# Performance work log

Hardware: AMD Instinct MI355X
Metric: run time of the kernel (lower is better)

The kernel has to match this reference:

```python
import jax, jax.numpy as jnp
import numpy as np

IN_CH = 64        # in_channels
MOD_H = 512       # modulation_hidden_dim
SIREN_H = 512     # siren_hidden_dim
NUM_PTS = 100
SCALE_INIT = 30.0  # SIREN first-layer frequency scale
N_STRANDS = 1024
NR_LAYERS = 3


def _wn_linear(x, v, g, b):
    # torch weight_norm(dim=0) on Linear: w = g * v / ||v||_row, row-wise over in-dim
    w = v * (g[:, None] / jnp.sqrt(jnp.sum(v * v, axis=1, keepdims=True)))
    return x @ w.T + b


def setup_inputs() -> dict:
    key = jax.random.key(0)
    ks = jax.random.split(key, 16)

    def p(k, shape, scale=0.05):
        return jax.random.normal(k, shape, dtype=jnp.float32) * scale

    inp = {"strand_features": p(ks[0], (N_STRANDS, IN_CH), 1.0)}
    mod_in = [IN_CH, MOD_H + IN_CH, MOD_H + IN_CH]
    for i in range(NR_LAYERS):
        inp[f"mod_v{i}"] = p(ks[1 + i], (MOD_H, mod_in[i]))
        inp[f"mod_g{i}"] = jnp.ones((MOD_H,), jnp.float32)
        inp[f"mod_b{i}"] = jnp.zeros((MOD_H,), jnp.float32)
    siren_in = [1, SIREN_H, SIREN_H]
    for i in range(NR_LAYERS):
        inp[f"siren_v{i}"] = p(ks[4 + i], (SIREN_H, siren_in[i]))
        inp[f"siren_g{i}"] = jnp.ones((SIREN_H,), jnp.float32)
        inp[f"siren_b{i}"] = jnp.zeros((SIREN_H,), jnp.float32)
    inp["dec_v"] = p(ks[7], (3, SIREN_H))
    inp["dec_g"] = jnp.ones((3,), jnp.float32)
    inp["dec_b"] = jnp.zeros((3,), jnp.float32)
    return inp


def reference(strand_features,
              mod_v0, mod_g0, mod_b0,
              mod_v1, mod_g1, mod_b1,
              mod_v2, mod_g2, mod_b2,
              siren_v0, siren_g0, siren_b0,
              siren_v1, siren_g1, siren_b1,
              siren_v2, siren_g2, siren_b2,
              dec_v, dec_g, dec_b):
    mods = [(mod_v0, mod_g0, mod_b0), (mod_v1, mod_g1, mod_b1), (mod_v2, mod_g2, mod_b2)]
    sirens = [(siren_v0, siren_g0, siren_b0), (siren_v1, siren_g1, siren_b1), (siren_v2, siren_g2, siren_b2)]

    n = strand_features.shape[0]
    nv = NUM_PTS - 1  # decode_random_verts=False, decode_direct_xyz=False
    # t = linspace(0,1,num_pts)[0:num_pts-1], shape (N, nv, 1)
    t = jnp.linspace(0.0, 1.0, NUM_PTS, dtype=jnp.float32)[:nv].reshape(1, nv, 1)
    h_siren = jnp.broadcast_to(t, (n, nv, 1))
    z_initial = jnp.broadcast_to(strand_features[:, None, :], (n, nv, IN_CH))  # z_scaling = 1.0
    z = z_initial
    for i in range(NR_LAYERS):
        h_mod = jax.nn.silu(_wn_linear(z, *mods[i]))       # (n, nv, MOD_H)
        s = _wn_linear(h_siren, *sirens[i])                # (n, nv, SIREN_H)
        s = jnp.sin(SCALE_INIT * s) if i == 0 else jnp.sin(s)
        h_siren = (1.0 - h_mod) * s                        # FiLM-style gating
        z = jnp.concatenate([z_initial, h_mod], axis=2)    # (n, nv, IN_CH+MOD_H)
    hair_dir = _wn_linear(h_siren, dec_v, dec_g, dec_b) * 0.01  # (n, nv, 3)
    pred = jnp.cumsum(hair_dir, axis=1)
    start = jnp.zeros((n, 1, 3), jnp.float32)
    return jnp.concatenate([start, pred], axis=1)  # (n, NUM_PTS, 3)
```

## Files before the change

### kernel.cpp

```cpp
#include <hip/hip_runtime.h>
#include <math.h>

#define NS 1024
#define NV 99
#define NPTS 100
#define H 512

typedef __bf16 bf16x8 __attribute__((ext_vector_type(8)));
typedef __bf16 bf16x4 __attribute__((ext_vector_type(4)));
typedef float f32x4 __attribute__((ext_vector_type(4)));

#define GLD_LDS16(gp, lp) __builtin_amdgcn_global_load_lds(                 \
    (const __attribute__((address_space(1))) void*)(gp),                    \
    (__attribute__((address_space(3))) void*)(lp), 16, 0, 0)
#define WAIT_VM0()   __builtin_amdgcn_s_waitcnt(0x0f70)
#define WAIT_LGKM0() __builtin_amdgcn_s_waitcnt(0xc07f)

__global__ __launch_bounds__(256) void k_wnorm(
    const float* __restrict__ mv0, const float* __restrict__ mg0,
    const float* __restrict__ mv1, const float* __restrict__ mg1,
    const float* __restrict__ mv2, const float* __restrict__ mg2,
    const float* __restrict__ sv0, const float* __restrict__ sg0,
    const float* __restrict__ sb0,
    const float* __restrict__ sv1, const float* __restrict__ sg1,
    const float* __restrict__ sv2, const float* __restrict__ sg2,
    const float* __restrict__ dv,  const float* __restrict__ dg,
    float* __restrict__ wnM0, float* __restrict__ wnM1, float* __restrict__ wnM2,
    __bf16* __restrict__ W1s, __bf16* __restrict__ W2s, float* __restrict__ wnD,
    float* __restrict__ s0sin)
{
    const int b = blockIdx.x, tid = threadIdx.x;
    if (b >= 641) {
        int idx = (b - 641) * 256 + tid;
        if (idx < NV * H) {
            int p = idx >> 9, j = idx & 511;
            float v = sv0[j];
            float w = sg0[j] * v * rsqrtf(v * v);
            float t = (float)p / 99.0f;
            s0sin[idx] = __sinf(30.0f * (t * w + sb0[j]));
        }
        return;
    }
    const int rid = b * 4 + (tid >> 6);
    const int lane = tid & 63;
    if (rid >= 2563) return;

    const float* src; const float* g; int len, j;
    float* dstf = nullptr; __bf16* dstb = nullptr;
    if (rid < 512)       { j = rid;        src = mv0 + j*64;  g = mg0; dstf = wnM0 + j*64;  len = 64;  }
    else if (rid < 1024) { j = rid - 512;  src = mv1 + j*576; g = mg1; dstf = wnM1 + j*576; len = 576; }
    else if (rid < 1536) { j = rid - 1024; src = mv2 + j*576; g = mg2; dstf = wnM2 + j*576; len = 576; }
    else if (rid < 2048) { j = rid - 1536; src = sv1 + j*512; g = sg1; dstb = W1s;          len = 512; }
    else if (rid < 2560) { j = rid - 2048; src = sv2 + j*512; g = sg2; dstb = W2s;          len = 512; }
    else                 { j = rid - 2560; src = dv  + j*512; g = dg;  dstf = wnD + j*512;  len = 512; }

    float ss = 0.f;
    for (int k = lane; k < len; k += 64) { float v = src[k]; ss += v * v; }
#pragma unroll
    for (int o = 1; o < 64; o <<= 1) ss += __shfl_xor(ss, o, 64);
    const float sc = g[j] * rsqrtf(ss);

    if (dstb) {
        for (int k = lane; k < len; k += 64) {
            int f  = (j >> 4) * 16 + (k >> 5);
            int el = ((f * 64) + ((k >> 3) & 3) * 16 + (j & 15)) * 8 + (k & 7);
            dstb[el] = (__bf16)(src[k] * sc);
        }
    } else {
        for (int k = lane; k < len; k += 64) dstf[k] = src[k] * sc;
    }
}

__global__ __launch_bounds__(256) void k_mod(
    const float* __restrict__ sf,
    const float* __restrict__ wnM0, const float* __restrict__ mb0,
    const float* __restrict__ wnM1, const float* __restrict__ mb1,
    const float* __restrict__ wnM2, const float* __restrict__ mb2,
    float* __restrict__ onem)
{
    const int g0 = blockIdx.x * 4, tid = threadIdx.x;
    __shared__ float z[4][576];

    for (int idx = tid; idx < 4 * 64; idx += 256)
        z[idx >> 6][idx & 63] = sf[(g0 + (idx >> 6)) * 64 + (idx & 63)];
    __syncthreads();

    float mreg[2][4];
#pragma unroll
    for (int r = 0; r < 2; ++r) {
        const int j = tid + 256 * r;
        const float* wr = wnM0 + j * 64;
        float acc[4] = {0.f, 0.f, 0.f, 0.f};
#pragma unroll
        for (int k = 0; k < 64; k += 4) {
            float4 w = *(const float4*)(wr + k);
#pragma unroll
            for (int g = 0; g < 4; ++g) {
                float4 zv = *(const float4*)&z[g][k];
                acc[g] += zv.x * w.x + zv.y * w.y + zv.z * w.z + zv.w * w.w;
            }
        }
        const float b = mb0[j];
#pragma unroll
        for (int g = 0; g < 4; ++g) {
            float a = acc[g] + b;
            float m = a / (1.f + __expf(-a));
            onem[(g0 + g) * H + j] = 1.f - m;
            mreg[r][g] = m;
        }
    }
    __syncthreads();
#pragma unroll
    for (int r = 0; r < 2; ++r)
#pragma unroll
        for (int g = 0; g < 4; ++g) z[g][64 + tid + 256 * r] = mreg[r][g];
    __syncthreads();

#pragma unroll
    for (int r = 0; r < 2; ++r) {
        const int j = tid + 256 * r;
        const float* wr = wnM1 + j * 576;
        float acc[4] = {0.f, 0.f, 0.f, 0.f};
        for (int k = 0; k < 576; k += 4) {
            float4 w = *(const float4*)(wr + k);
#pragma unroll
            for (int g = 0; g < 4; ++g) {
                float4 zv = *(const float4*)&z[g][k];
                acc[g] += zv.x * w.x + zv.y * w.y + zv.z * w.z + zv.w * w.w;
            }
        }
        const float b = mb1[j];
#pragma unroll
        for (int g = 0; g < 4; ++g) {
            float a = acc[g] + b;
            float m = a / (1.f + __expf(-a));
            onem[NS * H + (g0 + g) * H + j] = 1.f - m;
            mreg[r][g] = m;
        }
    }
    __syncthreads();
#pragma unroll
    for (int r = 0; r < 2; ++r)
#pragma unroll
        for (int g = 0; g < 4; ++g) z[g][64 + tid + 256 * r] = mreg[r][g];
    __syncthreads();

#pragma unroll
    for (int r = 0; r < 2; ++r) {
        const int j = tid + 256 * r;
        const float* wr = wnM2 + j * 576;
        float acc[4] = {0.f, 0.f, 0.f, 0.f};
        for (int k = 0; k < 576; k += 4) {
            float4 w = *(const float4*)(wr + k);
#pragma unroll
            for (int g = 0; g < 4; ++g) {
                float4 zv = *(const float4*)&z[g][k];
                acc[g] += zv.x * w.x + zv.y * w.y + zv.z * w.z + zv.w * w.w;
            }
        }
        const float b = mb2[j];
#pragma unroll
        for (int g = 0; g < 4; ++g) {
            float a = acc[g] + b;
            float m = a / (1.f + __expf(-a));
            onem[2 * NS * H + (g0 + g) * H + j] = 1.f - m;
        }
    }
}

__global__ __launch_bounds__(64, 1) void k_main(
    const __bf16* __restrict__ W1s, const __bf16* __restrict__ W2s,
    const float* __restrict__ wnD, const float* __restrict__ sb1,
    const float* __restrict__ sb2, const float* __restrict__ db,
    const float* __restrict__ s0sin, const float* __restrict__ onem,
    float* __restrict__ dirs)
{
    __shared__ __attribute__((aligned(16))) __bf16 h2p[32][520];
    __shared__ __attribute__((aligned(16))) __bf16 wst[8192];
    const int lane = threadIdx.x;
    const int L = lane & 15, Q = lane >> 4;
    const int base = blockIdx.x * 32;
    const int r0 = base + L, r1 = r0 + 16;
    const int s0 = r0 / 99, p0 = r0 - s0 * 99;
    const int s1 = r1 / 99, p1 = r1 - s1 * 99;

    bf16x8 Bh0[16], Bh1[16];
    {
        const float* omA = onem + s0 * H;
        const float* tsA = s0sin + p0 * H;
        const float* omB = onem + s1 * H;
        const float* tsB = s0sin + p1 * H;
#pragma unroll
        for (int t = 0; t < 16; ++t) {
            const int k0 = t * 32 + Q * 8;
            f32x4 oa = *(const f32x4*)(omA + k0);
            f32x4 ob = *(const f32x4*)(omA + k0 + 4);
            f32x4 ta = *(const f32x4*)(tsA + k0);
            f32x4 tb = *(const f32x4*)(tsA + k0 + 4);
            bf16x8 v;
            v[0] = (__bf16)(oa[0] * ta[0]); v[1] = (__bf16)(oa[1] * ta[1]);
            v[2] = (__bf16)(oa[2] * ta[2]); v[3] = (__bf16)(oa[3] * ta[3]);
            v[4] = (__bf16)(ob[0] * tb[0]); v[5] = (__bf16)(ob[1] * tb[1]);
            v[6] = (__bf16)(ob[2] * tb[2]); v[7] = (__bf16)(ob[3] * tb[3]);
            Bh0[t] = v;
            oa = *(const f32x4*)(omB + k0);
            ob = *(const f32x4*)(omB + k0 + 4);
            ta = *(const f32x4*)(tsB + k0);
            tb = *(const f32x4*)(tsB + k0 + 4);
            v[0] = (__bf16)(oa[0] * ta[0]); v[1] = (__bf16)(oa[1] * ta[1]);
            v[2] = (__bf16)(oa[2] * ta[2]); v[3] = (__bf16)(oa[3] * ta[3]);
            v[4] = (__bf16)(ob[0] * tb[0]); v[5] = (__bf16)(ob[1] * tb[1]);
            v[6] = (__bf16)(ob[2] * tb[2]); v[7] = (__bf16)(ob[3] * tb[3]);
            Bh1[t] = v;
        }
    }

    {
        const float* om1a = onem + NS * H + s0 * H;
        const float* om1b = onem + NS * H + s1 * H;
#pragma unroll 1
        for (int kb = 0; kb < 16; ++kb) {
            const __bf16* gpA = W1s + (size_t)kb * 16384 + (size_t)lane * 8;
            WAIT_LGKM0();
#pragma unroll
            for (int t = 0; t < 16; ++t)
                GLD_LDS16(gpA + t * 512, &wst[t * 512]);
            WAIT_VM0();
            f32x4 a00 = {0.f,0.f,0.f,0.f}, a01 = {0.f,0.f,0.f,0.f};
#pragma unroll
            for (int t = 0; t < 16; ++t) {
                bf16x8 w = *(const bf16x8*)&wst[t * 512 + lane * 8];
                a00 = __builtin_amdgcn_mfma_f32_16x16x32_bf16(w, Bh0[t], a00, 0, 0, 0);
                a01 = __builtin_amdgcn_mfma_f32_16x16x32_bf16(w, Bh1[t], a01, 0, 0, 0);
            }
            const __bf16* gpB = gpA + 16 * 512;
            WAIT_LGKM0();
#pragma unroll
            for (int t = 0; t < 16; ++t)
                GLD_LDS16(gpB + t * 512, &wst[t * 512]);
            WAIT_VM0();
            f32x4 a10 = {0.f,0.f,0.f,0.f}, a11 = {0.f,0.f,0.f,0.f};
#pragma unroll
            for (int t = 0; t < 16; ++t) {
                bf16x8 w = *(const bf16x8*)&wst[t * 512 + lane * 8];
                a10 = __builtin_amdgcn_mfma_f32_16x16x32_bf16(w, Bh0[t], a10, 0, 0, 0);
                a11 = __builtin_amdgcn_mfma_f32_16x16x32_bf16(w, Bh1[t], a11, 0, 0, 0);
            }
            const int c0 = kb * 32 + Q * 4, c1 = c0 + 16;
            float4 bi0 = *(const float4*)(sb1 + c0);
            float4 bi1 = *(const float4*)(sb1 + c1);
            float4 ga0 = *(const float4*)(om1a + c0);
            float4 ga1 = *(const float4*)(om1a + c1);
            float4 gb0 = *(const float4*)(om1b + c0);
            float4 gb1 = *(const float4*)(om1b + c1);
            bf16x4 v;
            v[0] = (__bf16)(ga0.x * __sinf(a00[0] + bi0.x));
            v[1] = (__bf16)(ga0.y * __sinf(a00[1] + bi0.y));
            v[2] = (__bf16)(ga0.z * __sinf(a00[2] + bi0.z));
            v[3] = (__bf16)(ga0.w * __sinf(a00[3] + bi0.w));
            *(bf16x4*)&h2p[L][c0] = v;
            v[0] = (__bf16)(ga1.x * __sinf(a10[0] + bi1.x));
            v[1] = (__bf16)(ga1.y * __sinf(a10[1] + bi1.y));
            v[2] = (__bf16)(ga1.z * __sinf(a10[2] + bi1.z));
            v[3] = (__bf16)(ga1.w * __sinf(a10[3] + bi1.w));
            *(bf16x4*)&h2p[L][c1] = v;
            v[0] = (__bf16)(gb0.x * __sinf(a01[0] + bi0.x));
            v[1] = (__bf16)(gb0.y * __sinf(a01[1] + bi0.y));
            v[2] = (__bf16)(gb0.z * __sinf(a01[2] + bi0.z));
            v[3] = (__bf16)(gb0.w * __sinf(a01[3] + bi0.w));
            *(bf16x4*)&h2p[16 + L][c0] = v;
            v[0] = (__bf16)(gb1.x * __sinf(a11[0] + bi1.x));
            v[1] = (__bf16)(gb1.y * __sinf(a11[1] + bi1.y));
            v[2] = (__bf16)(gb1.z * __sinf(a11[2] + bi1.z));
            v[3] = (__bf16)(gb1.w * __sinf(a11[3] + bi1.w));
            *(bf16x4*)&h2p[16 + L][c1] = v;
        }
    }
    __syncthreads();

#pragma unroll
    for (int t = 0; t < 16; ++t) {
        Bh0[t] = *(const bf16x8*)&h2p[L][t * 32 + Q * 8];
        Bh1[t] = *(const bf16x8*)&h2p[16 + L][t * 32 + Q * 8];
    }

    float pA0 = 0.f, pA1 = 0.f, pA2 = 0.f;
    float pB0 = 0.f, pB1 = 0.f, pB2 = 0.f;
    {
        const float* om2a = onem + 2 * NS * H + s0 * H;
        const float* om2b = onem + 2 * NS * H + s1 * H;
#pragma unroll 1
        for (int kb = 0; kb < 16; ++kb) {
            const __bf16* gpA = W2s + (size_t)kb * 16384 + (size_t)lane * 8;
            WAIT_LGKM0();
#pragma unroll
            for (int t = 0; t < 16; ++t)
                GLD_LDS16(gpA + t * 512, &wst[t * 512]);
            WAIT_VM0();
            f32x4 a00 = {0.f,0.f,0.f,0.f}, a01 = {0.f,0.f,0.f,0.f};
#pragma unroll
            for (int t = 0; t < 16; ++t) {
                bf16x8 w = *(const bf16x8*)&wst[t * 512 + lane * 8];
                a00 = __builtin_amdgcn_mfma_f32_16x16x32_bf16(w, Bh0[t], a00, 0, 0, 0);
                a01 = __builtin_amdgcn_mfma_f32_16x16x32_bf16(w, Bh1[t], a01, 0, 0, 0);
            }
            const __bf16* gpB = gpA + 16 * 512;
            WAIT_LGKM0();
#pragma unroll
            for (int t = 0; t < 16; ++t)
                GLD_LDS16(gpB + t * 512, &wst[t * 512]);
            WAIT_VM0();
            f32x4 a10 = {0.f,0.f,0.f,0.f}, a11 = {0.f,0.f,0.f,0.f};
#pragma unroll
            for (int t = 0; t < 16; ++t) {
                bf16x8 w = *(const bf16x8*)&wst[t * 512 + lane * 8];
                a10 = __builtin_amdgcn_mfma_f32_16x16x32_bf16(w, Bh0[t], a10, 0, 0, 0);
                a11 = __builtin_amdgcn_mfma_f32_16x16x32_bf16(w, Bh1[t], a11, 0, 0, 0);
            }
            const int c0 = kb * 32 + Q * 4, c1 = c0 + 16;
            float4 bi0 = *(const float4*)(sb2 + c0);
            float4 bi1 = *(const float4*)(sb2 + c1);
            float4 d00 = *(const float4*)(wnD + c0);
            float4 d10 = *(const float4*)(wnD + H + c0);
            float4 d20 = *(const float4*)(wnD + 2 * H + c0);
            float4 d01 = *(const float4*)(wnD + c1);
            float4 d11 = *(const float4*)(wnD + H + c1);
            float4 d21 = *(const float4*)(wnD + 2 * H + c1);
            float h;
            {
                float4 ga = *(const float4*)(om2a + c0);
                float4 gb = *(const float4*)(om2a + c1);
                h = ga.x * __sinf(a00[0] + bi0.x); pA0 += h * d00.x; pA1 += h * d10.x; pA2 += h * d20.x;
                h = ga.y * __sinf(a00[1] + bi0.y); pA0 += h * d00.y; pA1 += h * d10.y; pA2 += h * d20.y;
                h = ga.z * __sinf(a00[2] + bi0.z); pA0 += h * d00.z; pA1 += h * d10.z; pA2 += h * d20.z;
                h = ga.w * __sinf(a00[3] + bi0.w); pA0 += h * d00.w; pA1 += h * d10.w; pA2 += h * d20.w;
                h = gb.x * __sinf(a10[0] + bi1.x); pA0 += h * d01.x; pA1 += h * d11.x; pA2 += h * d21.x;
                h = gb.y * __sinf(a10[1] + bi1.y); pA0 += h * d01.y; pA1 += h * d11.y; pA2 += h * d21.y;
                h = gb.z * __sinf(a10[2] + bi1.z); pA0 += h * d01.z; pA1 += h * d11.z; pA2 += h * d21.z;
                h = gb.w * __sinf(a10[3] + bi1.w); pA0 += h * d01.w; pA1 += h * d11.w; pA2 += h * d21.w;
            }
            {
                float4 ga = *(const float4*)(om2b + c0);
                float4 gb = *(const float4*)(om2b + c1);
                h = ga.x * __sinf(a01[0] + bi0.x); pB0 += h * d00.x; pB1 += h * d10.x; pB2 += h * d20.x;
                h = ga.y * __sinf(a01[1] + bi0.y); pB0 += h * d00.y; pB1 += h * d10.y; pB2 += h * d20.y;
                h = ga.z * __sinf(a01[2] + bi0.z); pB0 += h * d00.z; pB1 += h * d10.z; pB2 += h * d20.z;
                h = ga.w * __sinf(a01[3] + bi0.w); pB0 += h * d00.w; pB1 += h * d10.w; pB2 += h * d20.w;
                h = gb.x * __sinf(a11[0] + bi1.x); pB0 += h * d01.x; pB1 += h * d11.x; pB2 += h * d21.x;
                h = gb.y * __sinf(a11[1] + bi1.y); pB0 += h * d01.y; pB1 += h * d11.y; pB2 += h * d21.y;
                h = gb.z * __sinf(a11[2] + bi1.z); pB0 += h * d01.z; pB1 += h * d11.z; pB2 += h * d21.z;
                h = gb.w * __sinf(a11[3] + bi1.w); pB0 += h * d01.w; pB1 += h * d11.w; pB2 += h * d21.w;
            }
        }
    }

    pA0 += __shfl_xor(pA0, 16, 64); pA0 += __shfl_xor(pA0, 32, 64);
    pA1 += __shfl_xor(pA1, 16, 64); pA1 += __shfl_xor(pA1, 32, 64);
    pA2 += __shfl_xor(pA2, 16, 64); pA2 += __shfl_xor(pA2, 32, 64);
    pB0 += __shfl_xor(pB0, 16, 64); pB0 += __shfl_xor(pB0, 32, 64);
    pB1 += __shfl_xor(pB1, 16, 64); pB1 += __shfl_xor(pB1, 32, 64);
    pB2 += __shfl_xor(pB2, 16, 64); pB2 += __shfl_xor(pB2, 32, 64);
    if (Q == 0) {
        const float d0 = db[0], d1 = db[1], d2 = db[2];
        dirs[r0 * 3 + 0] = 0.01f * (pA0 + d0);
        dirs[r0 * 3 + 1] = 0.01f * (pA1 + d1);
        dirs[r0 * 3 + 2] = 0.01f * (pA2 + d2);
        dirs[r1 * 3 + 0] = 0.01f * (pB0 + d0);
        dirs[r1 * 3 + 1] = 0.01f * (pB1 + d1);
        dirs[r1 * 3 + 2] = 0.01f * (pB2 + d2);
    }
}

__global__ __launch_bounds__(256) void k_cumsum(const float* __restrict__ dirs,
                                                float* __restrict__ out)
{
    const int wid = blockIdx.x * 4 + (threadIdx.x >> 6);
    const int lane = threadIdx.x & 63;
    const int s = wid / 3, c = wid - 3 * s;
    const float* dp = dirs + (size_t)s * NV * 3 + c;
    float v0 = dp[lane * 3];
    float v1 = (lane < NV - 64) ? dp[(64 + lane) * 3] : 0.f;
#pragma unroll
    for (int off = 1; off < 64; off <<= 1) {
        float t = __shfl_up(v0, off, 64);
        if (lane >= off) v0 += t;
        t = __shfl_up(v1, off, 64);
        if (lane >= off) v1 += t;
    }
    float tot0 = __shfl(v0, 63, 64);
    v1 += tot0;
    float* op = out + (size_t)s * NPTS * 3 + c;
    if (lane == 0) op[0] = 0.f;
    op[(lane + 1) * 3] = v0;
    if (lane < NV - 64) op[(64 + lane + 1) * 3] = v1;
}

extern "C" void kernel_launch(void* const* d_in, const int* in_sizes, int n_in,
                              void* d_out, int out_size, void* d_ws, size_t ws_size,
                              hipStream_t stream)
{
    const float* sf  = (const float*)d_in[0];
    const float* mv0 = (const float*)d_in[1];  const float* mg0 = (const float*)d_in[2];  const float* mb0 = (const float*)d_in[3];
    const float* mv1 = (const float*)d_in[4];  const float* mg1 = (const float*)d_in[5];  const float* mb1 = (const float*)d_in[6];
    const float* mv2 = (const float*)d_in[7];  const float* mg2 = (const float*)d_in[8];  const float* mb2 = (const float*)d_in[9];
    const float* sv0 = (const float*)d_in[10]; const float* sg0 = (const float*)d_in[11]; const float* sb0 = (const float*)d_in[12];
    const float* sv1 = (const float*)d_in[13]; const float* sg1 = (const float*)d_in[14]; const float* sb1 = (const float*)d_in[15];
    const float* sv2 = (const float*)d_in[16]; const float* sg2 = (const float*)d_in[17]; const float* sb2 = (const float*)d_in[18];
    const float* dv  = (const float*)d_in[19]; const float* dg  = (const float*)d_in[20]; const float* dbv = (const float*)d_in[21];

    float* ws = (float*)d_ws;
    float* wnM0  = ws;
    float* wnM1  = ws + 32768;
    float* wnM2  = ws + 327680;
    float* wnD   = ws + 622592;
    float* s0sin = ws + 624128;
    float* onem  = ws + 674816;
    float* dirs  = ws + 2247680;
    __bf16* W1s  = (__bf16*)(ws + 2551808);
    __bf16* W2s  = W1s + 262144;

    hipLaunchKernelGGL(k_wnorm, dim3(641 + 198), dim3(256), 0, stream,
                       mv0, mg0, mv1, mg1, mv2, mg2, sv0, sg0, sb0,
                       sv1, sg1, sv2, sg2, dv, dg,
                       wnM0, wnM1, wnM2, W1s, W2s, wnD, s0sin);
    hipLaunchKernelGGL(k_mod, dim3(256), dim3(256), 0, stream,
                       sf, wnM0, mb0, wnM1, mb1, wnM2, mb2, onem);
    hipLaunchKernelGGL(k_main, dim3((NS * NV) / 32), dim3(64), 0, stream,
                       W1s, W2s, wnD, sb1, sb2, dbv, s0sin, onem, dirs);
    hipLaunchKernelGGL(k_cumsum, dim3(768), dim3(256), 0, stream, dirs, (float*)d_out);
}
```

Baseline: 470.5 us.

## Stream SIREN weights through a 4-deep LDS ring with prefetch in k_main

After: 510.9 us. 1.09x slower.

```diff
diff --git a/kernel.cpp b/kernel.cpp
--- a/kernel.cpp
+++ b/kernel.cpp
@@ -5,6 +5,7 @@
 #define NV 99
 #define NPTS 100
 #define H 512
+#define CHUNK 2048
 
 typedef __bf16 bf16x8 __attribute__((ext_vector_type(8)));
 typedef __bf16 bf16x4 __attribute__((ext_vector_type(4)));
@@ -14,6 +15,7 @@
     (const __attribute__((address_space(1))) void*)(gp),                    \
     (__attribute__((address_space(3))) void*)(lp), 16, 0, 0)
 #define WAIT_VM0()   __builtin_amdgcn_s_waitcnt(0x0f70)
+#define WAIT_VM12()  __builtin_amdgcn_s_waitcnt(0x0f7c)
 #define WAIT_LGKM0() __builtin_amdgcn_s_waitcnt(0xc07f)
 
 __global__ __launch_bounds__(256) void k_wnorm(
@@ -46,11 +48,11 @@
     if (rid >= 2563) return;
 
     const float* src; const float* g; int len, j;
-    float* dstf = nullptr; __bf16* dstb = nullptr;
+    float* dstf = nullptr; __bf16* dstb = nullptr; bool perm = false;
     if (rid < 512)       { j = rid;        src = mv0 + j*64;  g = mg0; dstf = wnM0 + j*64;  len = 64;  }
     else if (rid < 1024) { j = rid - 512;  src = mv1 + j*576; g = mg1; dstf = wnM1 + j*576; len = 576; }
     else if (rid < 1536) { j = rid - 1024; src = mv2 + j*576; g = mg2; dstf = wnM2 + j*576; len = 576; }
-    else if (rid < 2048) { j = rid - 1536; src = sv1 + j*512; g = sg1; dstb = W1s;          len = 512; }
+    else if (rid < 2048) { j = rid - 1536; src = sv1 + j*512; g = sg1; dstb = W1s;          len = 512; perm = true; }
     else if (rid < 2560) { j = rid - 2048; src = sv2 + j*512; g = sg2; dstb = W2s;          len = 512; }
     else                 { j = rid - 2560; src = dv  + j*512; g = dg;  dstf = wnD + j*512;  len = 512; }
 
@@ -61,10 +63,19 @@
     const float sc = g[j] * rsqrtf(ss);
 
     if (dstb) {
-        for (int k = lane; k < len; k += 64) {
-            int f  = (j >> 4) * 16 + (k >> 5);
-            int el = ((f * 64) + ((k >> 3) & 3) * 16 + (j & 15)) * 8 + (k & 7);
-            dstb[el] = (__bf16)(src[k] * sc);
+        if (perm) {
+            const int ct = ((j >> 5) << 1) | ((j >> 2) & 1);
+            const int m  = (((j >> 3) & 3) << 2) | (j & 3);
+            for (int k = lane; k < len; k += 64) {
+                int el = ((ct * 16 + (k >> 5)) * 64 + ((k >> 3) & 3) * 16 + m) * 8 + (k & 7);
+                dstb[el] = (__bf16)(src[k] * sc);
+            }
+        } else {
+            for (int k = lane; k < len; k += 64) {
+                int f  = (j >> 4) * 16 + (k >> 5);
+                int el = ((f * 64) + ((k >> 3) & 3) * 16 + (j & 15)) * 8 + (k & 7);
+                dstb[el] = (__bf16)(src[k] * sc);
+            }
         }
     } else {
         for (int k = lane; k < len; k += 64) dstf[k] = src[k] * sc;
@@ -169,20 +180,28 @@
 }
 
 __global__ __launch_bounds__(64, 1) void k_main(
-    const __bf16* __restrict__ W1s, const __bf16* __restrict__ W2s,
+    const __bf16* __restrict__ Wstream, const __bf16* __restrict__ W2s_unused,
     const float* __restrict__ wnD, const float* __restrict__ sb1,
     const float* __restrict__ sb2, const float* __restrict__ db,
     const float* __restrict__ s0sin, const float* __restrict__ onem,
     float* __restrict__ dirs)
 {
-    __shared__ __attribute__((aligned(16))) __bf16 h2p[32][520];
-    __shared__ __attribute__((aligned(16))) __bf16 wst[8192];
+    __shared__ __attribute__((aligned(16))) __bf16 wst[4 * CHUNK];
+    __shared__ __attribute__((aligned(16))) __bf16 chs[32 * 512];
     const int lane = threadIdx.x;
     const int L = lane & 15, Q = lane >> 4;
     const int base = blockIdx.x * 32;
     const int r0 = base + L, r1 = r0 + 16;
     const int s0 = r0 / 99, p0 = r0 - s0 * 99;
     const int s1 = r1 / 99, p1 = r1 - s1 * 99;
+
+#pragma unroll
+    for (int c = 0; c < 3; ++c) {
+        const __bf16* gp = Wstream + c * CHUNK + lane * 8;
+#pragma unroll
+        for (int j = 0; j < 4; ++j)
+            GLD_LDS16(gp + j * 512, &wst[c * CHUNK + j * 512]);
+    }
 
     bf16x8 Bh0[16], Bh1[16];
     {
@@ -220,68 +239,69 @@
         const float* om1b = onem + NS * H + s1 * H;
 #pragma unroll 1
         for (int kb = 0; kb < 16; ++kb) {
-            const __bf16* gpA = W1s + (size_t)kb * 16384 + (size_t)lane * 8;
-            WAIT_LGKM0();
-#pragma unroll
-            for (int t = 0; t < 16; ++t)
-                GLD_LDS16(gpA + t * 512, &wst[t * 512]);
-            WAIT_VM0();
-            f32x4 a00 = {0.f,0.f,0.f,0.f}, a01 = {0.f,0.f,0.f,0.f};
-#pragma unroll
-            for (int t = 0; t < 16; ++t) {
-                bf16x8 w = *(const bf16x8*)&wst[t * 512 + lane * 8];
-                a00 = __builtin_amdgcn_mfma_f32_16x16x32_bf16(w, Bh0[t], a00, 0, 0, 0);
-                a01 = __builtin_amdgcn_mfma_f32_16x16x32_bf16(w, Bh1[t], a01, 0, 0, 0);
-            }
-            const __bf16* gpB = gpA + 16 * 512;
-            WAIT_LGKM0();
-#pragma unroll
-            for (int t = 0; t < 16; ++t)
-                GLD_LDS16(gpB + t * 512, &wst[t * 512]);
-            WAIT_VM0();
-            f32x4 a10 = {0.f,0.f,0.f,0.f}, a11 = {0.f,0.f,0.f,0.f};
-#pragma unroll
-            for (int t = 0; t < 16; ++t) {
-                bf16x8 w = *(const bf16x8*)&wst[t * 512 + lane * 8];
-                a10 = __builtin_amdgcn_mfma_f32_16x16x32_bf16(w, Bh0[t], a10, 0, 0, 0);
-                a11 = __builtin_amdgcn_mfma_f32_16x16x32_bf16(w, Bh1[t], a11, 0, 0, 0);
-            }
-            const int c0 = kb * 32 + Q * 4, c1 = c0 + 16;
-            float4 bi0 = *(const float4*)(sb1 + c0);
-            float4 bi1 = *(const float4*)(sb1 + c1);
-            float4 ga0 = *(const float4*)(om1a + c0);
-            float4 ga1 = *(const float4*)(om1a + c1);
-            float4 gb0 = *(const float4*)(om1b + c0);
-            float4 gb1 = *(const float4*)(om1b + c1);
-            bf16x4 v;
-            v[0] = (__bf16)(ga0.x * __sinf(a00[0] + bi0.x));
-            v[1] = (__bf16)(ga0.y * __sinf(a00[1] + bi0.y));
-            v[2] = (__bf16)(ga0.z * __sinf(a00[2] + bi0.z));
-            v[3] = (__bf16)(ga0.w * __sinf(a00[3] + bi0.w));
-            *(bf16x4*)&h2p[L][c0] = v;
-            v[0] = (__bf16)(ga1.x * __sinf(a10[0] + bi1.x));
-            v[1] = (__bf16)(ga1.y * __sinf(a10[1] + bi1.y));
-            v[2] = (__bf16)(ga1.z * __sinf(a10[2] + bi1.z));
-            v[3] = (__bf16)(ga1.w * __sinf(a10[3] + bi1.w));
-            *(bf16x4*)&h2p[L][c1] = v;
-            v[0] = (__bf16)(gb0.x * __sinf(a01[0] + bi0.x));
-            v[1] = (__bf16)(gb0.y * __sinf(a01[1] + bi0.y));
-            v[2] = (__bf16)(gb0.z * __sinf(a01[2] + bi0.z));
-            v[3] = (__bf16)(gb0.w * __sinf(a01[3] + bi0.w));
-            *(bf16x4*)&h2p[16 + L][c0] = v;
-            v[0] = (__bf16)(gb1.x * __sinf(a11[0] + bi1.x));
-            v[1] = (__bf16)(gb1.y * __sinf(a11[1] + bi1.y));
-            v[2] = (__bf16)(gb1.z * __sinf(a11[2] + bi1.z));
-            v[3] = (__bf16)(gb1.w * __sinf(a11[3] + bi1.w));
-            *(bf16x4*)&h2p[16 + L][c1] = v;
-        }
-    }
-    __syncthreads();
-
+            const int c = kb * 32 + Q * 8;
+            const float4 bi0 = *(const float4*)(sb1 + c);
+            const float4 bi1 = *(const float4*)(sb1 + c + 4);
+            const float4 gA0 = *(const float4*)(om1a + c);
+            const float4 gA1 = *(const float4*)(om1a + c + 4);
+            const float4 gB0 = *(const float4*)(om1b + c);
+            const float4 gB1 = *(const float4*)(om1b + c + 4);
+            f32x4 aA0 = {0.f,0.f,0.f,0.f}, aA1 = {0.f,0.f,0.f,0.f};
+            f32x4 aB0 = {0.f,0.f,0.f,0.f}, aB1 = {0.f,0.f,0.f,0.f};
+#pragma unroll
+            for (int sub = 0; sub < 8; ++sub) {
+                const int ck = kb * 8 + sub;
+                const int nc = (ck + 3) & 255;
+                WAIT_LGKM0();
+                {
+                    const __bf16* gp = Wstream + nc * CHUNK + lane * 8;
+                    __bf16* lp = &wst[(nc & 3) * CHUNK];
+#pragma unroll
+                    for (int j = 0; j < 4; ++j)
+                        GLD_LDS16(gp + j * 512, lp + j * 512);
+                }
+                WAIT_VM12();
+                const __bf16* rp = &wst[(ck & 3) * CHUNK + lane * 8];
+#pragma unroll
+                for (int t4 = 0; t4 < 4; ++t4) {
+                    bf16x8 w = *(const bf16x8*)(rp + t4 * 512);
+                    const int tt = (sub & 3) * 4 + t4;
+                    if (sub < 4) {
+                        aA0 = __builtin_amdgcn_mfma_f32_16x16x32_bf16(w, Bh0[tt], aA0, 0, 0, 0);
+                        aA1 = __builtin_amdgcn_mfma_f32_16x16x32_bf16(w, Bh1[tt], aA1, 0, 0, 0);
+                    } else {
+                        aB0 = __builtin_amdgcn_mfma_f32_16x16x32_bf16(w, Bh0[tt], aB0, 0, 0, 0);
+                        aB1 = __builtin_amdgcn_mfma_f32_16x16x32_bf16(w, Bh1[tt], aB1, 0, 0, 0);
+                    }
+                }
+            }
+            bf16x8 v;
+            v[0] = (__bf16)(gA0.x * __sinf(aA0[0] + bi0.x));
+            v[1] = (__bf16)(gA0.y * __sinf(aA0[1] + bi0.y));
+            v[2] = (__bf16)(gA0.z * __sinf(aA0[2] + bi0.z));
+            v[3] = (__bf16)(gA0.w * __sinf(aA0[3] + bi0.w));
+            v[4] = (__bf16)(gA1.x * __sinf(aB0[0] + bi1.x));
+            v[5] = (__bf16)(gA1.y * __sinf(aB0[1] + bi1.y));
+            v[6] = (__bf16)(gA1.z * __sinf(aB0[2] + bi1.z));
+            v[7] = (__bf16)(gA1.w * __sinf(aB0[3] + bi1.w));
+            *(bf16x8*)&chs[(kb * 64 + lane) * 8] = v;
+            v[0] = (__bf16)(gB0.x * __sinf(aA1[0] + bi0.x));
+            v[1] = (__bf16)(gB0.y * __sinf(aA1[1] + bi0.y));
+            v[2] = (__bf16)(gB0.z * __sinf(aA1[2] + bi0.z));
+            v[3] = (__bf16)(gB0.w * __sinf(aA1[3] + bi0.w));
+            v[4] = (__bf16)(gB1.x * __sinf(aB1[0] + bi1.x));
+            v[5] = (__bf16)(gB1.y * __sinf(aB1[1] + bi1.y));
+            v[6] = (__bf16)(gB1.z * __sinf(aB1[2] + bi1.z));
+            v[7] = (__bf16)(gB1.w * __sinf(aB1[3] + bi1.w));
+            *(bf16x8*)&chs[((16 + kb) * 64 + lane) * 8] = v;
+        }
+    }
+
+    WAIT_LGKM0();
 #pragma unroll
     for (int t = 0; t < 16; ++t) {
-        Bh0[t] = *(const bf16x8*)&h2p[L][t * 32 + Q * 8];
-        Bh1[t] = *(const bf16x8*)&h2p[16 + L][t * 32 + Q * 8];
+        Bh0[t] = *(const bf16x8*)&chs[(t * 64 + lane) * 8];
+        Bh1[t] = *(const bf16x8*)&chs[((16 + t) * 64 + lane) * 8];
     }
 
     float pA0 = 0.f, pA1 = 0.f, pA2 = 0.f;
@@ -291,66 +311,65 @@
         const float* om2b = onem + 2 * NS * H + s1 * H;
 #pragma unroll 1
         for (int kb = 0; kb < 16; ++kb) {
-            const __bf16* gpA = W2s + (size_t)kb * 16384 + (size_t)lane * 8;
-            WAIT_LGKM0();
-#pragma unroll
-            for (int t = 0; t < 16; ++t)
-                GLD_LDS16(gpA + t * 512, &wst[t * 512]);
-            WAIT_VM0();
-            f32x4 a00 = {0.f,0.f,0.f,0.f}, a01 = {0.f,0.f,0.f,0.f};
-#pragma unroll
-            for (int t = 0; t < 16; ++t) {
-                bf16x8 w = *(const bf16x8*)&wst[t * 512 + lane * 8];
-                a00 = __builtin_amdgcn_mfma_f32_16x16x32_bf16(w, Bh0[t], a00, 0, 0, 0);
-                a01 = __builtin_amdgcn_mfma_f32_16x16x32_bf16(w, Bh1[t], a01, 0, 0, 0);
-            }
-            const __bf16* gpB = gpA + 16 * 512;
-            WAIT_LGKM0();
-#pragma unroll
-            for (int t = 0; t < 16; ++t)
-                GLD_LDS16(gpB + t * 512, &wst[t * 512]);
-            WAIT_VM0();
-            f32x4 a10 = {0.f,0.f,0.f,0.f}, a11 = {0.f,0.f,0.f,0.f};
-#pragma unroll
-            for (int t = 0; t < 16; ++t) {
-                bf16x8 w = *(const bf16x8*)&wst[t * 512 + lane * 8];
-                a10 = __builtin_amdgcn_mfma_f32_16x16x32_bf16(w, Bh0[t], a10, 0, 0, 0);
-                a11 = __builtin_amdgcn_mfma_f32_16x16x32_bf16(w, Bh1[t], a11, 0, 0, 0);
-            }
             const int c0 = kb * 32 + Q * 4, c1 = c0 + 16;
-            float4 bi0 = *(const float4*)(sb2 + c0);
-            float4 bi1 = *(const float4*)(sb2 + c1);
-            float4 d00 = *(const float4*)(wnD + c0);
-            float4 d10 = *(const float4*)(wnD + H + c0);
-            float4 d20 = *(const float4*)(wnD + 2 * H + c0);
-            float4 d01 = *(const float4*)(wnD + c1);
-            float4 d11 = *(const float4*)(wnD + H + c1);
-            float4 d21 = *(const float4*)(wnD + 2 * H + c1);
+            const float4 bi0 = *(const float4*)(sb2 + c0);
+            const float4 bi1 = *(const float4*)(sb2 + c1);
+            const float4 d00 = *(const float4*)(wnD + c0);
+            const float4 d10 = *(const float4*)(wnD + H + c0);
+            const float4 d20 = *(const float4*)(wnD + 2 * H + c0);
+            const float4 d01 = *(const float4*)(wnD + c1);
+            const float4 d11 = *(const float4*)(wnD + H + c1);
+            const float4 d21 = *(const float4*)(wnD + 2 * H + c1);
+            const float4 ga0 = *(const float4*)(om2a + c0);
+            const float4 ga1 = *(const float4*)(om2a + c1);
+            const float4 gb0 = *(const float4*)(om2b + c0);
+            const float4 gb1 = *(const float4*)(om2b + c1);
+            f32x4 aA0 = {0.f,0.f,0.f,0.f}, aA1 = {0.f,0.f,0.f,0.f};
+            f32x4 aB0 = {0.f,0.f,0.f,0.f}, aB1 = {0.f,0.f,0.f,0.f};
+#pragma unroll
+            for (int sub = 0; sub < 8; ++sub) {
+                const int ck = 128 + kb * 8 + sub;
+                const int nc = (ck + 3) & 255;
+                WAIT_LGKM0();
+                {
+                    const __bf16* gp = Wstream + nc * CHUNK + lane * 8;
+                    __bf16* lp = &wst[(nc & 3) * CHUNK];
+#pragma unroll
+                    for (int j = 0; j < 4; ++j)
+                        GLD_LDS16(gp + j * 512, lp + j * 512);
+                }
+                WAIT_VM12();
+                const __bf16* rp = &wst[(ck & 3) * CHUNK + lane * 8];
+#pragma unroll
+                for (int t4 = 0; t4 < 4; ++t4) {
+                    bf16x8 w = *(const bf16x8*)(rp + t4 * 512);
+                    const int tt = (sub & 3) * 4 + t4;
+                    if (sub < 4) {
+                        aA0 = __builtin_amdgcn_mfma_f32_16x16x32_bf16(w, Bh0[tt], aA0, 0, 0, 0);
+                        aA1 = __builtin_amdgcn_mfma_f32_16x16x32_bf16(w, Bh1[tt], aA1, 0, 0, 0);
+                    } else {
+                        aB0 = __builtin_amdgcn_mfma_f32_16x16x32_bf16(w, Bh0[tt], aB0, 0, 0, 0);
+                        aB1 = __builtin_amdgcn_mfma_f32_16x16x32_bf16(w, Bh1[tt], aB1, 0, 0, 0);
+                    }
+                }
+            }
             float h;
-            {
-                float4 ga = *(const float4*)(om2a + c0);
-                float4 gb = *(const float4*)(om2a + c1);
-                h = ga.x * __sinf(a00[0] + bi0.x); pA0 += h * d00.x; pA1 += h * d10.x; pA2 += h * d20.x;
-                h = ga.y * __sinf(a00[1] + bi0.y); pA0 += h * d00.y; pA1 += h * d10.y; pA2 += h * d20.y;
-                h = ga.z * __sinf(a00[2] + bi0.z); pA0 += h * d00.z; pA1 += h * d10.z; pA2 += h * d20.z;
-                h = ga.w * __sinf(a00[3] + bi0.w); pA0 += h * d00.w; pA1 += h * d10.w; pA2 += h * d20.w;
-                h = gb.x * __sinf(a10[0] + bi1.x); pA0 += h * d01.x; pA1 += h * d11.x; pA2 += h * d21.x;
-                h = gb.y * __sinf(a10[1] + bi1.y); pA0 += h * d01.y; pA1 += h * d11.y; pA2 += h * d21.y;
-                h = gb.z * __sinf(a10[2] + bi1.z); pA0 += h * d01.z; pA1 += h * d11.z; pA2 += h * d21.z;
-                h = gb.w * __sinf(a10[3] + bi1.w); pA0 += h * d01.w; pA1 += h * d11.w; pA2 += h * d21.w;
-            }
-            {
-                float4 ga = *(const float4*)(om2b + c0);
-                float4 gb = *(const float4*)(om2b + c1);
-                h = ga.x * __sinf(a01[0] + bi0.x); pB0 += h * d00.x; pB1 += h * d10.x; pB2 += h * d20.x;
-                h = ga.y * __sinf(a01[1] + bi0.y); pB0 += h * d00.y; pB1 += h * d10.y; pB2 += h * d20.y;
-                h = ga.z * __sinf(a01[2] + bi0.z); pB0 += h * d00.z; pB1 += h * d10.z; pB2 += h * d20.z;
-                h = ga.w * __sinf(a01[3] + bi0.w); pB0 += h * d00.w; pB1 += h * d10.w; pB2 += h * d20.w;
-                h = gb.x * __sinf(a11[0] + bi1.x); pB0 += h * d01.x; pB1 += h * d11.x; pB2 += h * d21.x;
-                h = gb.y * __sinf(a11[1] + bi1.y); pB0 += h * d01.y; pB1 += h * d11.y; pB2 += h * d21.y;
-                h = gb.z * __sinf(a11[2] + bi1.z); pB0 += h * d01.z; pB1 += h * d11.z; pB2 += h * d21.z;
-                h = gb.w * __sinf(a11[3] + bi1.w); pB0 += h * d01.w; pB1 += h * d11.w; pB2 += h * d21.w;
-            }
+            h = ga0.x * __sinf(aA0[0] + bi0.x); pA0 += h * d00.x; pA1 += h * d10.x; pA2 += h * d20.x;
+            h = ga0.y * __sinf(aA0[1] + bi0.y); pA0 += h * d00.y; pA1 += h * d10.y; pA2 += h * d20.y;
+            h = ga0.z * __sinf(aA0[2] + bi0.z); pA0 += h * d00.z; pA1 += h * d10.z; pA2 += h * d20.z;
+            h = ga0.w * __sinf(aA0[3] + bi0.w); pA0 += h * d00.w; pA1 += h * d10.w; pA2 += h * d20.w;
+            h = ga1.x * __sinf(aB0[0] + bi1.x); pA0 += h * d01.x; pA1 += h * d11.x; pA2 += h * d21.x;
+            h = ga1.y * __sinf(aB0[1] + bi1.y); pA0 += h * d01.y; pA1 += h * d11.y; pA2 += h * d21.y;
+            h = ga1.z * __sinf(aB0[2] + bi1.z); pA0 += h * d01.z; pA1 += h * d11.z; pA2 += h * d21.z;
+            h = ga1.w * __sinf(aB0[3] + bi1.w); pA0 += h * d01.w; pA1 += h * d11.w; pA2 += h * d21.w;
+            h = gb0.x * __sinf(aA1[0] + bi0.x); pB0 += h * d00.x; pB1 += h * d10.x; pB2 += h * d20.x;
+            h = gb0.y * __sinf(aA1[1] + bi0.y); pB0 += h * d00.y; pB1 += h * d10.y; pB2 += h * d20.y;
+            h = gb0.z * __sinf(aA1[2] + bi0.z); pB0 += h * d00.z; pB1 += h * d10.z; pB2 += h * d20.z;
+            h = gb0.w * __sinf(aA1[3] + bi0.w); pB0 += h * d00.w; pB1 += h * d10.w; pB2 += h * d20.w;
+            h = gb1.x * __sinf(aB1[0] + bi1.x); pB0 += h * d01.x; pB1 += h * d11.x; pB2 += h * d21.x;
+            h = gb1.y * __sinf(aB1[1] + bi1.y); pB0 += h * d01.y; pB1 += h * d11.y; pB2 += h * d21.y;
+            h = gb1.z * __sinf(aB1[2] + bi1.z); pB0 += h * d01.z; pB1 += h * d11.z; pB2 += h * d21.z;
+            h = gb1.w * __sinf(aB1[3] + bi1.w); pB0 += h * d01.w; pB1 += h * d11.w; pB2 += h * d21.w;
         }
     }
 
```
